# Kernel tuning notes

Measured on AMD Instinct MI355X. Metric: run time of the kernel, lower is better.

The kernel has to match this reference:

```python
import jax, jax.numpy as jnp
import numpy as np

BETA = 0.25
EPS_NORM = 1e-12   # matches torch F.normalize eps
EPS_COS = 1e-6     # clamp floor for cos weight


def _l2_normalize(v, axis=-1):
    n = jnp.linalg.norm(v, axis=axis, keepdims=True)
    return v / jnp.maximum(n, EPS_NORM)


def setup_inputs() -> dict:
    key = jax.random.key(0)
    kx, kc = jax.random.split(key)
    x = jax.random.normal(kx, (64, 1024, 256), dtype=jnp.float32)
    codebook = jax.random.normal(kc, (4096, 256), dtype=jnp.float32)
    return {"x": x, "codebook": codebook}


def reference(x, codebook):
    # Normalize codebook rows (F.normalize(codebook, dim=-1)).
    cb_n = _l2_normalize(codebook)                     # [K, D]
    # Cosine distance: 1 - cos_sim(x, cb). Only sim matters for argmin.
    x_n = _l2_normalize(x)                             # [B, S, D]
    sim = jnp.einsum('bsd,kd->bsk', x_n, cb_n)         # [B, S, K]
    dists = 1.0 - sim
    ids = jnp.argmin(dists, axis=-1)                   # [B, S] int
    c_k = cb_n[ids]                                    # [B, S, D] gather
    # Cosine weight uses RAW x (x_norm = x in the torch code).
    cos_k = jnp.sum(x * c_k, axis=-1, keepdims=True)   # [B, S, 1]
    cos_k = jnp.maximum(cos_k, EPS_COS)
    weighted_emb = cos_k * c_k                         # [B, S, D]
    # Cosine quantization loss: codebook term + beta * commitment term,
    # each 1 - cos_sim with stop-gradient on the opposite operand.
    def cos_sim(a, b):
        return jnp.sum(_l2_normalize(a) * _l2_normalize(b), axis=-1)
    codebook_term = jnp.mean(1.0 - cos_sim(jax.lax.stop_gradient(x), c_k))
    commit_term = jnp.mean(1.0 - cos_sim(x, jax.lax.stop_gradient(c_k)))
    loss = codebook_term + BETA * commit_term
    return ids, weighted_emb, loss
```

## Files before the change

### kernel.cpp

```cpp
#include <hip/hip_runtime.h>
#include <math.h>
#include <stdint.h>


#define TOKENS 65536
#define DIM 256
#define KCB 4096

#define TB 256
#define DELTA_SCALE 0.03125f
#define LIST_CAP (1u << 21)
#define SCAP 4096

typedef short bf16x8 __attribute__((ext_vector_type(8)));
typedef float f32x4 __attribute__((ext_vector_type(4)));

__device__ inline short f2bf(float f) {
    uint32_t u = __float_as_uint(f);
    u += 0x7FFF + ((u >> 16) & 1);
    return (short)(u >> 16);
}

__global__ void prep_all(const float* __restrict__ cb, const float* __restrict__ x,
                         float* __restrict__ cbn, short* __restrict__ cbh2,
                         float* __restrict__ xnorm, float* __restrict__ invnx) {
    int bid  = blockIdx.x;
    int w    = threadIdx.x >> 6;
    int lane = threadIdx.x & 63;
    if (bid < KCB / 4) {
        int row = bid * 4 + w;
        float4 v = *(const float4*)(cb + (size_t)row * DIM + lane * 4);
        float ss = v.x * v.x + v.y * v.y + v.z * v.z + v.w * v.w;
#pragma unroll
        for (int off = 32; off; off >>= 1) ss += __shfl_xor(ss, off);
        float scale = 1.0f / fmaxf(sqrtf(ss), 1e-12f);
        float4 o = {v.x * scale, v.y * scale, v.z * scale, v.w * scale};
        *(float4*)(cbn + (size_t)row * DIM + lane * 4) = o;
        short4 h = {f2bf(o.x), f2bf(o.y), f2bf(o.z), f2bf(o.w)};
        int g = row >> 4, l15 = row & 15;
        int kst = lane >> 3, q = (lane >> 1) & 3, jhalf = lane & 1;
        size_t dst = ((size_t)((g * 8 + kst) * 64 + q * 16 + l15)) * 8 + jhalf * 4;
        *(short4*)(cbh2 + dst) = h;
    } else {
        int row = (bid - KCB / 4) * 4 + w;
        float4 v = *(const float4*)(x + (size_t)row * DIM + lane * 4);
        float ss = v.x * v.x + v.y * v.y + v.z * v.z + v.w * v.w;
#pragma unroll
        for (int off = 32; off; off >>= 1) ss += __shfl_xor(ss, off);
        if (lane == 0) {
            float n = fmaxf(sqrtf(ss), 1e-12f);
            xnorm[row] = n;
            invnx[row] = 1.0f / n;
        }
    }
}

__global__ __launch_bounds__(512, 2) void mfma_select(
    const float* __restrict__ x, const short* __restrict__ cbh2,
    const float* __restrict__ xnorm,
    uint32_t* __restrict__ list, uint32_t* __restrict__ cnt) {
    __shared__ uint32_t s_list[SCAP];
    __shared__ uint32_t s_cnt, s_base;
    __shared__ float maxbuf[2][TB];

    const int tid  = threadIdx.x;
    const int lane = tid & 63;
    const int wid  = tid >> 6;
    const int tq   = wid >> 1;
    const int ch   = wid & 1;
    const int l15  = lane & 15, q = lane >> 4;
    const int tb   = blockIdx.x * TB;
    const int twb  = tb + tq * 64;

    if (tid == 0) s_cnt = 0;

    bf16x8 areg[4][8];
#pragma unroll
    for (int mf = 0; mf < 4; ++mf) {
        const float* xr = x + (size_t)(twb + mf * 16 + l15) * DIM + q * 8;
#pragma unroll
        for (int kst = 0; kst < 8; ++kst) {
            float4 f0 = *(const float4*)(xr + kst * 32);
            float4 f1 = *(const float4*)(xr + kst * 32 + 4);
            bf16x8 h;
            h[0] = f2bf(f0.x); h[1] = f2bf(f0.y); h[2] = f2bf(f0.z); h[3] = f2bf(f0.w);
            h[4] = f2bf(f1.x); h[5] = f2bf(f1.y); h[6] = f2bf(f1.z); h[7] = f2bf(f1.w);
            areg[mf][kst] = h;
        }
    }

    float rmax[4][4];
#pragma unroll
    for (int mf = 0; mf < 4; ++mf)
#pragma unroll
        for (int r = 0; r < 4; ++r) rmax[mf][r] = -3.0e38f;

    for (int ct = 0; ct < 128; ++ct) {
        const short* bp = cbh2 + (size_t)(ch * 128 + ct) * 4096 + lane * 8;
        bf16x8 b[8];
#pragma unroll
        for (int j = 0; j < 8; ++j) b[j] = *(const bf16x8*)(bp + j * 512);
        __builtin_amdgcn_sched_barrier(0);
        f32x4 acc[4];
#pragma unroll
        for (int mf = 0; mf < 4; ++mf) acc[mf] = (f32x4){0.f, 0.f, 0.f, 0.f};
#pragma unroll
        for (int kst = 0; kst < 8; ++kst)
#pragma unroll
            for (int mf = 0; mf < 4; ++mf)
                acc[mf] = __builtin_amdgcn_mfma_f32_16x16x32_bf16(
                    areg[mf][kst], b[kst], acc[mf], 0, 0, 0);
#pragma unroll
        for (int mf = 0; mf < 4; ++mf)
#pragma unroll
            for (int r = 0; r < 4; ++r)
                rmax[mf][r] = fmaxf(rmax[mf][r], acc[mf][r]);
    }

#pragma unroll
    for (int mf = 0; mf < 4; ++mf)
#pragma unroll
        for (int r = 0; r < 4; ++r) {
            float v = rmax[mf][r];
#pragma unroll
            for (int o = 1; o < 16; o <<= 1) v = fmaxf(v, __shfl_xor(v, o));
            rmax[mf][r] = v;
        }
    if (l15 == 0) {
#pragma unroll
        for (int mf = 0; mf < 4; ++mf)
#pragma unroll
            for (int r = 0; r < 4; ++r)
                maxbuf[ch][tq * 64 + mf * 16 + q * 4 + r] = rmax[mf][r];
    }
    __syncthreads();
    float thr[4][4];
#pragma unroll
    for (int mf = 0; mf < 4; ++mf)
#pragma unroll
        for (int r = 0; r < 4; ++r) {
            int tl = tq * 64 + mf * 16 + q * 4 + r;
            thr[mf][r] = fmaxf(maxbuf[0][tl], maxbuf[1][tl])
                       - DELTA_SCALE * xnorm[tb + tl];
        }

    for (int ct = 0; ct < 128; ++ct) {
        const short* bp = cbh2 + (size_t)(ch * 128 + ct) * 4096 + lane * 8;
        bf16x8 b[8];
#pragma unroll
        for (int j = 0; j < 8; ++j) b[j] = *(const bf16x8*)(bp + j * 512);
        __builtin_amdgcn_sched_barrier(0);
        f32x4 acc[4];
#pragma unroll
        for (int mf = 0; mf < 4; ++mf) acc[mf] = (f32x4){0.f, 0.f, 0.f, 0.f};
#pragma unroll
        for (int kst = 0; kst < 8; ++kst)
#pragma unroll
            for (int mf = 0; mf < 4; ++mf)
                acc[mf] = __builtin_amdgcn_mfma_f32_16x16x32_bf16(
                    areg[mf][kst], b[kst], acc[mf], 0, 0, 0);
#pragma unroll
        for (int mf = 0; mf < 4; ++mf)
#pragma unroll
            for (int r = 0; r < 4; ++r) {
                if (acc[mf][r] >= thr[mf][r]) {
                    uint32_t t = twb + mf * 16 + q * 4 + r;
                    uint32_t c = ch * 2048 + ct * 16 + l15;
                    uint32_t e = (t << 12) | c;
                    uint32_t idx = atomicAdd(&s_cnt, 1u);
                    if (idx < SCAP) {
                        s_list[idx] = e;
                    } else {
                        uint32_t g2 = atomicAdd(cnt, 1u);
                        if (g2 < LIST_CAP) list[g2] = e;
                    }
                }
            }
    }

    __syncthreads();
    if (tid == 0) {
        uint32_t m = s_cnt;
        if (m > SCAP) m = SCAP;
        s_base = atomicAdd(cnt, m);
        s_cnt = m;
    }
    __syncthreads();
    for (uint32_t i = tid; i < s_cnt; i += 512) {
        uint32_t idx = s_base + i;
        if (idx < LIST_CAP) list[idx] = s_list[i];
    }
}

__global__ void rescore(const float* __restrict__ x, const float* __restrict__ cbn,
                        const float* __restrict__ invnx,
                        const uint32_t* __restrict__ list, const uint32_t* __restrict__ cnt,
                        unsigned long long* __restrict__ win) {
    uint32_t n = *cnt;
    if (n > LIST_CAP) n = LIST_CAP;
    for (uint32_t e = blockIdx.x * blockDim.x + threadIdx.x; e < n;
         e += gridDim.x * blockDim.x) {
        uint32_t v = list[e];
        uint32_t t = v >> 12, c = v & 4095;
        const float* xp = x + (size_t)t * DIM;
        const float* cp = cbn + (size_t)c * DIM;
        float acc = 0.0f;
#pragma unroll 8
        for (int k = 0; k < DIM; ++k) acc = fmaf(xp[k], cp[k], acc);
        float s = acc * invnx[t];
        float dist = 1.0f - s;
        uint32_t u = __float_as_uint(dist);
        u = (u & 0x80000000u) ? ~u : (u | 0x80000000u);
        unsigned long long key = ((unsigned long long)u << 32) | c;
        atomicMin(win + t, key);
    }
}

__global__ void epilogue_kernel(const float* __restrict__ x, const float* __restrict__ cbn,
                                const float* __restrict__ invnx,
                                const unsigned long long* __restrict__ win,
                                float* __restrict__ ids_f,
                                float* __restrict__ emb, float* __restrict__ partials) {
    int w    = threadIdx.x >> 6;
    int lane = threadIdx.x & 63;
    int t    = blockIdx.x * 4 + w;
    int id   = (int)(win[t] & 0xFFFFFFFFull);
    if ((unsigned)id > 4095u) id = 0;
    if (lane == 0) ids_f[t] = (float)id;

    float4 c4 = *(const float4*)(cbn + (size_t)id * DIM + lane * 4);
    float4 x4 = *(const float4*)(x + (size_t)t * DIM + lane * 4);
    float dxc = c4.x * x4.x + c4.y * x4.y + c4.z * x4.z + c4.w * x4.w;
    float ssc = c4.x * c4.x + c4.y * c4.y + c4.z * c4.z + c4.w * c4.w;
#pragma unroll
    for (int off = 32; off; off >>= 1) {
        dxc += __shfl_xor(dxc, off);
        ssc += __shfl_xor(ssc, off);
    }
    float cosk = fmaxf(dxc, 1e-6f);
    float4 o = {cosk * c4.x, cosk * c4.y, cosk * c4.z, cosk * c4.w};
    *(float4*)(emb + (size_t)t * DIM + lane * 4) = o;

    float invnc = 1.0f / fmaxf(sqrtf(ssc), 1e-12f);
    float term = 1.0f - dxc * invnx[t] * invnc;

    __shared__ float sterm[4];
    if (lane == 0) sterm[w] = term;
    __syncthreads();
    if (threadIdx.x == 0)
        partials[blockIdx.x] = sterm[0] + sterm[1] + sterm[2] + sterm[3];
}

__global__ void finalize_kernel(const float* __restrict__ partials, float* __restrict__ loss) {
    __shared__ float buf[256];
    float s = 0.0f;
    for (int i = threadIdx.x; i < TOKENS / 4; i += 256) s += partials[i];
    buf[threadIdx.x] = s;
    __syncthreads();
    for (int st = 128; st; st >>= 1) {
        if (threadIdx.x < st) buf[threadIdx.x] += buf[threadIdx.x + st];
        __syncthreads();
    }
    if (threadIdx.x == 0) loss[0] = buf[0] * (1.25f / (float)TOKENS);
}

extern "C" void kernel_launch(void* const* d_in, const int* in_sizes, int n_in,
                              void* d_out, int out_size, void* d_ws, size_t ws_size,
                              hipStream_t stream) {
    const float* x  = (const float*)d_in[0];
    const float* cb = (const float*)d_in[1];

    float* out   = (float*)d_out;
    float* ids_f = out;
    float* emb   = out + TOKENS;
    float* loss  = out + TOKENS + (size_t)TOKENS * DIM;

    float* ws = (float*)d_ws;
    float* cbn   = ws;
    short* cbh2  = (short*)(cbn + (size_t)KCB * DIM);
    float* xnorm = (float*)(cbh2 + (size_t)KCB * DIM);
    float* invnx = xnorm + TOKENS;
    unsigned long long* win = (unsigned long long*)(invnx + TOKENS);
    uint32_t* list = (uint32_t*)(win + TOKENS);
    uint32_t* cnt  = list + LIST_CAP;
    float* partials = (float*)(cnt + 16);

    hipMemsetAsync(cnt, 0, 64, stream);
    hipMemsetAsync(win, 0xFF, sizeof(unsigned long long) * TOKENS, stream);

    prep_all<<<KCB / 4 + TOKENS / 4, 256, 0, stream>>>(cb, x, cbn, cbh2, xnorm, invnx);
    mfma_select<<<TOKENS / TB, 512, 0, stream>>>(x, cbh2, xnorm, list, cnt);
    rescore<<<1024, 256, 0, stream>>>(x, cbn, invnx, list, cnt, win);
    epilogue_kernel<<<TOKENS / 4, 256, 0, stream>>>(x, cbn, invnx, win, ids_f, emb, partials);
    finalize_kernel<<<1, 256, 0, stream>>>(partials, loss);
}
```

Baseline: 435.1 us.

## Fuse candidate collection into first pass with running-max threshold, shrink second pass

The first GEMM pass now keeps a running per-token max, refreshes a threshold every 16 codebook tiles, and emits candidates on the fly once past the first 16 tiles. The second full GEMM pass shrinks to only the first 16 tiles, re-checked against the final threshold. This removes most of the redundant second-pass MFMA work, at the cost of emitting more candidates, because the running threshold is looser than the final one. To compensate, the shared candidate buffer is enlarged and the rescore loop is vectorized with float4 loads.

```diff
diff --git a/kernel.cpp b/kernel.cpp
--- a/kernel.cpp
+++ b/kernel.cpp
@@ -10,7 +10,8 @@
 #define TB 256
 #define DELTA_SCALE 0.03125f
 #define LIST_CAP (1u << 21)
-#define SCAP 4096
+#define SCAP 6144
+#define PRIME 16
 
 typedef short bf16x8 __attribute__((ext_vector_type(8)));
 typedef float f32x4 __attribute__((ext_vector_type(4)));
@@ -89,13 +90,33 @@
         }
     }
 
-    float rmax[4][4];
+    float xnd[4][4];
 #pragma unroll
     for (int mf = 0; mf < 4; ++mf)
 #pragma unroll
-        for (int r = 0; r < 4; ++r) rmax[mf][r] = -3.0e38f;
+        for (int r = 0; r < 4; ++r)
+            xnd[mf][r] = DELTA_SCALE * xnorm[twb + mf * 16 + q * 4 + r];
+
+    __syncthreads();
+
+    float rmax[4][4], thrv[4][4];
+#pragma unroll
+    for (int mf = 0; mf < 4; ++mf)
+#pragma unroll
+        for (int r = 0; r < 4; ++r) { rmax[mf][r] = -3.0e38f; thrv[mf][r] = 3.0e38f; }
 
     for (int ct = 0; ct < 128; ++ct) {
+        if ((ct & 15) == 0 && ct) {
+#pragma unroll
+            for (int mf = 0; mf < 4; ++mf)
+#pragma unroll
+                for (int r = 0; r < 4; ++r) {
+                    float v = rmax[mf][r];
+#pragma unroll
+                    for (int o = 1; o < 16; o <<= 1) v = fmaxf(v, __shfl_xor(v, o));
+                    thrv[mf][r] = v - xnd[mf][r];
+                }
+        }
         const short* bp = cbh2 + (size_t)(ch * 128 + ct) * 4096 + lane * 8;
         bf16x8 b[8];
 #pragma unroll
@@ -110,6 +131,21 @@
             for (int mf = 0; mf < 4; ++mf)
                 acc[mf] = __builtin_amdgcn_mfma_f32_16x16x32_bf16(
                     areg[mf][kst], b[kst], acc[mf], 0, 0, 0);
+        if (ct >= PRIME) {
+#pragma unroll
+            for (int mf = 0; mf < 4; ++mf)
+#pragma unroll
+                for (int r = 0; r < 4; ++r) {
+                    if (acc[mf][r] >= thrv[mf][r]) {
+                        uint32_t t = twb + mf * 16 + q * 4 + r;
+                        uint32_t c = ch * 2048 + ct * 16 + l15;
+                        uint32_t e = (t << 12) | c;
+                        uint32_t idx = atomicAdd(&s_cnt, 1u);
+                        if (idx < SCAP) s_list[idx] = e;
+                        else { uint32_t g2 = atomicAdd(cnt, 1u); if (g2 < LIST_CAP) list[g2] = e; }
+                    }
+                }
+        }
 #pragma unroll
         for (int mf = 0; mf < 4; ++mf)
 #pragma unroll
@@ -140,11 +176,10 @@
 #pragma unroll
         for (int r = 0; r < 4; ++r) {
             int tl = tq * 64 + mf * 16 + q * 4 + r;
-            thr[mf][r] = fmaxf(maxbuf[0][tl], maxbuf[1][tl])
-                       - DELTA_SCALE * xnorm[tb + tl];
-        }
-
-    for (int ct = 0; ct < 128; ++ct) {
+            thr[mf][r] = fmaxf(maxbuf[0][tl], maxbuf[1][tl]) - xnd[mf][r];
+        }
+
+    for (int ct = 0; ct < PRIME; ++ct) {
         const short* bp = cbh2 + (size_t)(ch * 128 + ct) * 4096 + lane * 8;
         bf16x8 b[8];
 #pragma unroll
@@ -168,12 +203,8 @@
                     uint32_t c = ch * 2048 + ct * 16 + l15;
                     uint32_t e = (t << 12) | c;
                     uint32_t idx = atomicAdd(&s_cnt, 1u);
-                    if (idx < SCAP) {
-                        s_list[idx] = e;
-                    } else {
-                        uint32_t g2 = atomicAdd(cnt, 1u);
-                        if (g2 < LIST_CAP) list[g2] = e;
-                    }
+                    if (idx < SCAP) s_list[idx] = e;
+                    else { uint32_t g2 = atomicAdd(cnt, 1u); if (g2 < LIST_CAP) list[g2] = e; }
                 }
             }
     }
@@ -202,11 +233,18 @@
          e += gridDim.x * blockDim.x) {
         uint32_t v = list[e];
         uint32_t t = v >> 12, c = v & 4095;
-        const float* xp = x + (size_t)t * DIM;
-        const float* cp = cbn + (size_t)c * DIM;
+        const float4* xp = (const float4*)(x + (size_t)t * DIM);
+        const float4* cp = (const float4*)(cbn + (size_t)c * DIM);
         float acc = 0.0f;
 #pragma unroll 8
-        for (int k = 0; k < DIM; ++k) acc = fmaf(xp[k], cp[k], acc);
+        for (int k = 0; k < DIM / 4; ++k) {
+            float4 xv = xp[k];
+            float4 cv = cp[k];
+            acc = fmaf(xv.x, cv.x, acc);
+            acc = fmaf(xv.y, cv.y, acc);
+            acc = fmaf(xv.z, cv.z, acc);
+            acc = fmaf(xv.w, cv.w, acc);
+        }
         float s = acc * invnx[t];
         float dist = 1.0f - s;
         uint32_t u = __float_as_uint(dist);
```

Result: slower. 702.8 us (+61.5%).
